# Performance work log

Hardware: AMD Instinct MI355X
Metric: run time of the kernel (lower is better)

## Reference

```python
import jax, jax.numpy as jnp
import numpy as np

N, D = 16384, 16
EPS = 1e-15
SQRT_C = 1.0            # curvature c = 1 Poincare ball
MAX_NORM = (1.0 - 1e-5) / SQRT_C
ATANH_CLIP = 1.0 - 1e-7


def _proj(x):
    # clip points to stay strictly inside the Poincare ball
    norm = jnp.maximum(jnp.linalg.norm(x, axis=-1, keepdims=True), EPS)
    scale = jnp.where(norm > MAX_NORM, MAX_NORM / norm, 1.0)
    return x * scale


def _logmap0(x):
    # log map at the origin: artanh(sqrt(c)|x|) * x / (sqrt(c)|x|)
    norm = jnp.maximum(jnp.linalg.norm(x, axis=-1, keepdims=True), EPS)
    arg = jnp.minimum(SQRT_C * norm, ATANH_CLIP)
    return jnp.arctanh(arg) * x / (SQRT_C * norm)


def _expmap0(u):
    # exp map at the origin: tanh(sqrt(c)|u|) * u / (sqrt(c)|u|)
    norm = jnp.maximum(jnp.linalg.norm(u, axis=-1, keepdims=True), EPS)
    return jnp.tanh(SQRT_C * norm) * u / (SQRT_C * norm)


def setup_inputs() -> dict:
    key = jax.random.key(0)
    kx, ka = jax.random.split(key)
    # node embeddings strictly inside the unit ball
    x = 0.3 * jax.random.normal(kx, (N, D), dtype=jnp.float32)
    x = _proj(x)
    # dense non-negative adjacency, row-normalized (mean aggregation)
    adj = jax.random.uniform(ka, (N, N), dtype=jnp.float32)
    adj = adj / jnp.sum(adj, axis=-1, keepdims=True)
    return {"x": x, "adj": adj}


def reference(x, adj):
    x_tangent = _logmap0(x)                 # [N, D] pointwise transcendental
    res = jnp.matmul(adj, x_tangent)        # [N, N] @ [N, D] aggregation
    return _proj(_expmap0(res))             # map back to manifold + project
```

## Files before the change

### kernel.cpp

```cpp
#include <hip/hip_runtime.h>
#include <math.h>

#define NROWS 16384
#define DIM   16
#define KC    1024
#define WGT   512
#define RPW   4
#define RPWG  32

static __device__ __forceinline__ void fma4(float4& a, float s, const float4& b) {
    a.x = fmaf(s, b.x, a.x);
    a.y = fmaf(s, b.y, a.y);
    a.z = fmaf(s, b.z, a.z);
    a.w = fmaf(s, b.w, a.w);
}

static __device__ __forceinline__ float dot4(const float4& a) {
    return a.x * a.x + a.y * a.y + a.z * a.z + a.w * a.w;
}

static __device__ __forceinline__ float4 scale4(const float4& a, float s) {
    return make_float4(a.x * s, a.y * s, a.z * s, a.w * s);
}

__global__ void hyp_logmap0(const float* __restrict__ x, float* __restrict__ xt) {
    int row = blockIdx.x * blockDim.x + threadIdx.x;
    const float4* src = (const float4*)(x + (size_t)row * DIM);
    float4 q0 = src[0], q1 = src[1], q2 = src[2], q3 = src[3];
    float n2 = dot4(q0) + dot4(q1) + dot4(q2) + dot4(q3);
    float n  = fmaxf(sqrtf(n2), 1e-15f);
    float arg = fminf(n, 1.0f - 1e-7f);
    float f = atanhf(arg) / n;
    float4* dst = (float4*)(xt + (size_t)row * DIM);
    dst[0] = scale4(q0, f);
    dst[1] = scale4(q1, f);
    dst[2] = scale4(q2, f);
    dst[3] = scale4(q3, f);
}

__global__ __launch_bounds__(WGT, 4) void hyp_agg(
        const float* __restrict__ adj, const float* __restrict__ xt,
        float* __restrict__ out) {
    __shared__ float4 planes[4][KC];

    const int tid  = threadIdx.x;
    const int lane = tid & 63;
    const int wave = tid >> 6;
    const int rowBase = blockIdx.x * RPWG + wave * RPW;

    const float* a0 = adj + (size_t)(rowBase + 0) * NROWS;
    const float* a1 = adj + (size_t)(rowBase + 1) * NROWS;
    const float* a2 = adj + (size_t)(rowBase + 2) * NROWS;
    const float* a3 = adj + (size_t)(rowBase + 3) * NROWS;

    float4 acc[RPW][4];
#pragma unroll
    for (int r = 0; r < RPW; ++r)
#pragma unroll
        for (int j = 0; j < 4; ++j)
            acc[r][j] = make_float4(0.f, 0.f, 0.f, 0.f);

    for (int kc = 0; kc < NROWS; kc += KC) {
        __syncthreads();
#pragma unroll
        for (int kk = tid; kk < KC; kk += WGT) {
            const float4* src = (const float4*)(xt + (size_t)(kc + kk) * DIM);
            float4 q0 = src[0], q1 = src[1], q2 = src[2], q3 = src[3];
            planes[0][kk] = q0;
            planes[1][kk] = q1;
            planes[2][kk] = q2;
            planes[3][kk] = q3;
        }
        __syncthreads();

#pragma unroll 2
        for (int it = 0; it < KC / 64; ++it) {
            const int kk = it * 64 + lane;
            const int k  = kc + kk;
            float v0 = __builtin_nontemporal_load(a0 + k);
            float v1 = __builtin_nontemporal_load(a1 + k);
            float v2 = __builtin_nontemporal_load(a2 + k);
            float v3 = __builtin_nontemporal_load(a3 + k);
            float4 q0 = planes[0][kk];
            float4 q1 = planes[1][kk];
            float4 q2 = planes[2][kk];
            float4 q3 = planes[3][kk];
            fma4(acc[0][0], v0, q0); fma4(acc[0][1], v0, q1);
            fma4(acc[0][2], v0, q2); fma4(acc[0][3], v0, q3);
            fma4(acc[1][0], v1, q0); fma4(acc[1][1], v1, q1);
            fma4(acc[1][2], v1, q2); fma4(acc[1][3], v1, q3);
            fma4(acc[2][0], v2, q0); fma4(acc[2][1], v2, q1);
            fma4(acc[2][2], v2, q2); fma4(acc[2][3], v2, q3);
            fma4(acc[3][0], v3, q0); fma4(acc[3][1], v3, q1);
            fma4(acc[3][2], v3, q2); fma4(acc[3][3], v3, q3);
        }
    }

#pragma unroll
    for (int r = 0; r < RPW; ++r) {
#pragma unroll
        for (int j = 0; j < 4; ++j) {
            float4 v = acc[r][j];
#pragma unroll
            for (int m = 1; m < 64; m <<= 1) {
                v.x += __shfl_xor(v.x, m, 64);
                v.y += __shfl_xor(v.y, m, 64);
                v.z += __shfl_xor(v.z, m, 64);
                v.w += __shfl_xor(v.w, m, 64);
            }
            acc[r][j] = v;
        }
    }

#pragma unroll
    for (int r = 0; r < RPW; ++r) {
        float4 s0 = acc[r][0], s1 = acc[r][1], s2 = acc[r][2], s3 = acc[r][3];
        float n2 = dot4(s0) + dot4(s1) + dot4(s2) + dot4(s3);
        float n  = fmaxf(sqrtf(n2), 1e-15f);
        float t  = tanhf(n);
        float fac = t / n;
        float ny = fmaxf(sqrtf(n2) * fac, 1e-15f);
        const float MAX_NORM = 1.0f - 1e-5f;
        float sc = (ny > MAX_NORM) ? (MAX_NORM / ny) : 1.0f;
        float tot = fac * sc;
        if (lane == 0) {
            float4* dst = (float4*)(out + (size_t)(rowBase + r) * DIM);
            dst[0] = scale4(s0, tot);
            dst[1] = scale4(s1, tot);
            dst[2] = scale4(s2, tot);
            dst[3] = scale4(s3, tot);
        }
    }
}

extern "C" void kernel_launch(void* const* d_in, const int* in_sizes, int n_in,
                              void* d_out, int out_size, void* d_ws, size_t ws_size,
                              hipStream_t stream) {
    const float* x   = (const float*)d_in[0];
    const float* adj = (const float*)d_in[1];
    float* out = (float*)d_out;
    float* xt  = (float*)d_ws;

    hipLaunchKernelGGL(hyp_logmap0, dim3(NROWS / 256), dim3(256), 0, stream, x, xt);
    hipLaunchKernelGGL(hyp_agg, dim3(NROWS / RPWG), dim3(WGT), 0, stream, adj, xt, out);
}
```

Before: 224.4 us.

## Double-buffer xt tiles via global_load_lds and vectorize adjacency loads

The tangent features are now written in a strided plane layout, so each chunk can be copied straight into LDS with global_load_lds into a double buffer, letting the next chunk's staging overlap the current chunk's compute. The chunk size is halved to fit two buffers. Adjacency rows are read as float4 per lane instead of scalars, giving wider memory transactions, and each loaded vector is consumed against four feature sub-planes. The final norm after tanh is simplified to reuse t directly. The layout change couples both kernels and adds a dependence on correct async LDS copy semantics.

New measurement: 231.3 us. 1.03x slower.

```diff
diff --git a/kernel.cpp b/kernel.cpp
--- a/kernel.cpp
+++ b/kernel.cpp
@@ -3,10 +3,14 @@
 
 #define NROWS 16384
 #define DIM   16
-#define KC    1024
+#define KC    512
+#define NCH   (NROWS / KC)
 #define WGT   512
 #define RPW   4
 #define RPWG  32
+#define NT4   (NROWS / 4)
+
+typedef float vfloat4 __attribute__((ext_vector_type(4)));
 
 static __device__ __forceinline__ void fma4(float4& a, float s, const float4& b) {
     a.x = fmaf(s, b.x, a.x);
@@ -14,34 +18,34 @@
     a.z = fmaf(s, b.z, a.z);
     a.w = fmaf(s, b.w, a.w);
 }
-
 static __device__ __forceinline__ float dot4(const float4& a) {
     return a.x * a.x + a.y * a.y + a.z * a.z + a.w * a.w;
 }
-
 static __device__ __forceinline__ float4 scale4(const float4& a, float s) {
     return make_float4(a.x * s, a.y * s, a.z * s, a.w * s);
 }
 
-__global__ void hyp_logmap0(const float* __restrict__ x, float* __restrict__ xt) {
-    int row = blockIdx.x * blockDim.x + threadIdx.x;
+__global__ void hyp_logmap0(const float* __restrict__ x, float4* __restrict__ xtp) {
+    int tid = blockIdx.x * blockDim.x + threadIdx.x;
+    int s = tid >> 12;
+    int t = tid & (NT4 - 1);
+    int row = 4 * t + s;
     const float4* src = (const float4*)(x + (size_t)row * DIM);
     float4 q0 = src[0], q1 = src[1], q2 = src[2], q3 = src[3];
     float n2 = dot4(q0) + dot4(q1) + dot4(q2) + dot4(q3);
     float n  = fmaxf(sqrtf(n2), 1e-15f);
     float arg = fminf(n, 1.0f - 1e-7f);
     float f = atanhf(arg) / n;
-    float4* dst = (float4*)(xt + (size_t)row * DIM);
-    dst[0] = scale4(q0, f);
-    dst[1] = scale4(q1, f);
-    dst[2] = scale4(q2, f);
-    dst[3] = scale4(q3, f);
+    xtp[(0 * 4 + s) * NT4 + t] = scale4(q0, f);
+    xtp[(1 * 4 + s) * NT4 + t] = scale4(q1, f);
+    xtp[(2 * 4 + s) * NT4 + t] = scale4(q2, f);
+    xtp[(3 * 4 + s) * NT4 + t] = scale4(q3, f);
 }
 
 __global__ __launch_bounds__(WGT, 4) void hyp_agg(
-        const float* __restrict__ adj, const float* __restrict__ xt,
+        const float* __restrict__ adj, const float4* __restrict__ xtp,
         float* __restrict__ out) {
-    __shared__ float4 planes[4][KC];
+    __shared__ float4 planes[2][16][KC / 4];
 
     const int tid  = threadIdx.x;
     const int lane = tid & 63;
@@ -60,40 +64,57 @@
         for (int j = 0; j < 4; ++j)
             acc[r][j] = make_float4(0.f, 0.f, 0.f, 0.f);
 
-    for (int kc = 0; kc < NROWS; kc += KC) {
-        __syncthreads();
+    auto stage = [&](int buf, int kc) {
 #pragma unroll
-        for (int kk = tid; kk < KC; kk += WGT) {
-            const float4* src = (const float4*)(xt + (size_t)(kc + kk) * DIM);
-            float4 q0 = src[0], q1 = src[1], q2 = src[2], q3 = src[3];
-            planes[0][kk] = q0;
-            planes[1][kk] = q1;
-            planes[2][kk] = q2;
-            planes[3][kk] = q3;
+        for (int i = 0; i < 4; ++i) {
+            const int idx = wave * 4 + i;
+            const int p   = idx >> 1;
+            const int h   = idx & 1;
+            const float4* src = xtp + (size_t)p * NT4 + (kc >> 2) + h * 64 + lane;
+            __builtin_amdgcn_global_load_lds(
+                (const __attribute__((address_space(1))) void*)src,
+                (__attribute__((address_space(3))) void*)&planes[buf][p][h * 64],
+                16, 0, 0);
+        }
+    };
+
+    stage(0, 0);
+    __syncthreads();
+
+    for (int c = 0; c < NCH; ++c) {
+        const int kc  = c * KC;
+        const int buf = c & 1;
+        if (c + 1 < NCH) stage(buf ^ 1, kc + KC);
+
+#pragma unroll
+        for (int it = 0; it < KC / 256; ++it) {
+            const int col = kc + it * 256 + 4 * lane;
+            vfloat4 v0 = __builtin_nontemporal_load((const vfloat4*)(a0 + col));
+            vfloat4 v1 = __builtin_nontemporal_load((const vfloat4*)(a1 + col));
+            vfloat4 v2 = __builtin_nontemporal_load((const vfloat4*)(a2 + col));
+            vfloat4 v3 = __builtin_nontemporal_load((const vfloat4*)(a3 + col));
+#pragma unroll
+            for (int s = 0; s < 4; ++s) {
+                const int t = it * 64 + lane;
+                float4 q0 = planes[buf][0 * 4 + s][t];
+                float4 q1 = planes[buf][1 * 4 + s][t];
+                float4 q2 = planes[buf][2 * 4 + s][t];
+                float4 q3 = planes[buf][3 * 4 + s][t];
+                float c0 = v0[s];
+                float c1 = v1[s];
+                float c2 = v2[s];
+                float c3 = v3[s];
+                fma4(acc[0][0], c0, q0); fma4(acc[0][1], c0, q1);
+                fma4(acc[0][2], c0, q2); fma4(acc[0][3], c0, q3);
+                fma4(acc[1][0], c1, q0); fma4(acc[1][1], c1, q1);
+                fma4(acc[1][2], c1, q2); fma4(acc[1][3], c1, q3);
+                fma4(acc[2][0], c2, q0); fma4(acc[2][1], c2, q1);
+                fma4(acc[2][2], c2, q2); fma4(acc[2][3], c2, q3);
+                fma4(acc[3][0], c3, q0); fma4(acc[3][1], c3, q1);
+                fma4(acc[3][2], c3, q2); fma4(acc[3][3], c3, q3);
+            }
         }
         __syncthreads();
-
-#pragma unroll 2
-        for (int it = 0; it < KC / 64; ++it) {
-            const int kk = it * 64 + lane;
-            const int k  = kc + kk;
-            float v0 = __builtin_nontemporal_load(a0 + k);
-            float v1 = __builtin_nontemporal_load(a1 + k);
-            float v2 = __builtin_nontemporal_load(a2 + k);
-            float v3 = __builtin_nontemporal_load(a3 + k);
-            float4 q0 = planes[0][kk];
-            float4 q1 = planes[1][kk];
-            float4 q2 = planes[2][kk];
-            float4 q3 = planes[3][kk];
-            fma4(acc[0][0], v0, q0); fma4(acc[0][1], v0, q1);
-            fma4(acc[0][2], v0, q2); fma4(acc[0][3], v0, q3);
-            fma4(acc[1][0], v1, q0); fma4(acc[1][1], v1, q1);
-            fma4(acc[1][2], v1, q2); fma4(acc[1][3], v1, q3);
-            fma4(acc[2][0], v2, q0); fma4(acc[2][1], v2, q1);
-            fma4(acc[2][2], v2, q2); fma4(acc[2][3], v2, q3);
-            fma4(acc[3][0], v3, q0); fma4(acc[3][1], v3, q1);
-            fma4(acc[3][2], v3, q2); fma4(acc[3][3], v3, q3);
-        }
     }
 
 #pragma unroll
@@ -119,9 +140,9 @@
         float n  = fmaxf(sqrtf(n2), 1e-15f);
         float t  = tanhf(n);
         float fac = t / n;
-        float ny = fmaxf(sqrtf(n2) * fac, 1e-15f);
+        float ny  = fmaxf(t, 1e-15f);
         const float MAX_NORM = 1.0f - 1e-5f;
-        float sc = (ny > MAX_NORM) ? (MAX_NORM / ny) : 1.0f;
+        float sc  = (ny > MAX_NORM) ? (MAX_NORM / ny) : 1.0f;
         float tot = fac * sc;
         if (lane == 0) {
             float4* dst = (float4*)(out + (size_t)(rowBase + r) * DIM);
@@ -138,9 +159,9 @@
                               hipStream_t stream) {
     const float* x   = (const float*)d_in[0];
     const float* adj = (const float*)d_in[1];
-    float* out = (float*)d_out;
-    float* xt  = (float*)d_ws;
+    float* out  = (float*)d_out;
+    float4* xtp = (float4*)d_ws;
 
-    hipLaunchKernelGGL(hyp_logmap0, dim3(NROWS / 256), dim3(256), 0, stream, x, xt);
-    hipLaunchKernelGGL(hyp_agg, dim3(NROWS / RPWG), dim3(WGT), 0, stream, adj, xt, out);
+    hipLaunchKernelGGL(hyp_logmap0, dim3(NROWS / 256), dim3(256), 0, stream, x, xtp);
+    hipLaunchKernelGGL(hyp_agg, dim3(NROWS / RPWG), dim3(WGT), 0, stream, adj, xtp, out);
 }
```
